# Kernel optimization log

Measured on AMD Instinct MI355X. Metric: run time of the kernel, lower is better.

Reference implementation:

```python
import jax, jax.numpy as jnp
import numpy as np

H = 1024
N_HEAD = 16
HEAD = H // N_HEAD
EPS = 1e-12


def setup_inputs() -> dict:
    key = jax.random.key(0)
    ks = jax.random.split(key, 12)
    B, S = 2, 2048
    scale = 1.0 / np.sqrt(H)
    inp = {
        "pre_out": jax.random.normal(ks[0], (B, S, H), dtype=jnp.float32),
        "att_mask": jnp.ones((B, 1, 1, S), dtype=jnp.float32),
        "Wq": jax.random.normal(ks[1], (H, H), dtype=jnp.float32) * scale,
        "bq": jnp.zeros((H,), dtype=jnp.float32),
        "Wk": jax.random.normal(ks[2], (H, H), dtype=jnp.float32) * scale,
        "bk": jnp.zeros((H,), dtype=jnp.float32),
        "Wv": jax.random.normal(ks[3], (H, H), dtype=jnp.float32) * scale,
        "bv": jnp.zeros((H,), dtype=jnp.float32),
        "Wo": jax.random.normal(ks[4], (H, H), dtype=jnp.float32) * scale,
        "bo": jnp.zeros((H,), dtype=jnp.float32),
        "ln_w": jnp.ones((H,), dtype=jnp.float32),
        "ln_b": jnp.zeros((H,), dtype=jnp.float32),
    }
    return inp


def _heads(x):
    # [B,S,H] -> [B,n_head,S,head]
    B, S, _ = x.shape
    return x.reshape(B, S, N_HEAD, HEAD).transpose(0, 2, 1, 3)


def _layernorm(x, w, b):
    u = jnp.mean(x, axis=-1, keepdims=True)
    s = jnp.mean((x - u) ** 2, axis=-1, keepdims=True)
    return w * ((x - u) / jnp.sqrt(s + EPS)) + b


def reference(pre_out, att_mask, Wq, bq, Wk, bk, Wv, bv, Wo, bo, ln_w, ln_b):
    B, S, _ = pre_out.shape
    # torch Linear: y = x @ W.T + b
    Q = _heads(pre_out @ Wq.T + bq)
    K = _heads(pre_out @ Wk.T + bk)
    V = _heads(pre_out @ Wv.T + bv)
    scores = jnp.einsum('bhqd,bhkd->bhqk', Q, K) / np.sqrt(HEAD)
    scores = scores + (1.0 - att_mask) * -10000.0
    prob = jax.nn.softmax(scores, axis=-1)  # eval mode: no dropout
    att = jnp.einsum('bhqk,bhkd->bhqd', prob, V)
    att = att.transpose(0, 2, 1, 3).reshape(B, S, H)
    out = att @ Wo.T + bo
    return _layernorm(pre_out + out, ln_w, ln_b)
```

## Files before the change

### kernel.cpp

```cpp
#include <hip/hip_runtime.h>
#include <math.h>

typedef unsigned short u16;
typedef float floatx4 __attribute__((ext_vector_type(4)));
typedef __bf16 bf16x8 __attribute__((ext_vector_type(8)));
typedef u16 u16x4 __attribute__((ext_vector_type(4)));

#define BB 2
#define SS 2048
#define HH 1024
#define NHEAD 16

__device__ __forceinline__ u16 f2bf(float f) {
  union { float f; unsigned u; } a; a.f = f;
  unsigned r = a.u + 0x7fffu + ((a.u >> 16) & 1u);
  return (u16)(r >> 16);
}

__device__ __forceinline__ u16 bfbits(float f) {
  union { __bf16 h; u16 u; } c; c.h = (__bf16)f; return c.u;
}

__device__ __forceinline__ unsigned cvtpk(float lo, float hi) {
  unsigned r;
  asm("v_cvt_pk_bf16_f32 %0, %1, %2" : "=v"(r) : "v"(lo), "v"(hi));
  return r;
}

__device__ __forceinline__ void gload16(const u16* g, u16* l) {
  __builtin_amdgcn_global_load_lds((const __attribute__((address_space(1))) void*)g,
                                   (__attribute__((address_space(3))) void*)l, 16, 0, 0);
}

__device__ __forceinline__ void fencebar() {
  asm volatile("" ::: "memory");
  __builtin_amdgcn_s_barrier();
  asm volatile("" ::: "memory");
}

__global__ __launch_bounds__(256) void cvt_all(
    const float* __restrict__ X, const float* __restrict__ Wq, const float* __restrict__ Wk,
    const float* __restrict__ Wv, const float* __restrict__ Wo, const float* __restrict__ mask,
    u16* __restrict__ Xb, u16* __restrict__ Wqb, u16* __restrict__ Wkb,
    u16* __restrict__ Wvb, u16* __restrict__ Wob, float* __restrict__ B2) {
  int i = blockIdx.x * 256 + threadIdx.x;
  if (i >= (2 << 20)) {
    int off = i - (2 << 20);
    float4 m = ((const float4*)mask)[off];
    float4 o;
    o.x = (1.0f - m.x) * (-10000.0f * 1.44269504f);
    o.y = (1.0f - m.y) * (-10000.0f * 1.44269504f);
    o.z = (1.0f - m.z) * (-10000.0f * 1.44269504f);
    o.w = (1.0f - m.w) * (-10000.0f * 1.44269504f);
    ((float4*)B2)[off] = o;
    return;
  }
  const float* src; u16* dst; int off;
  if (i < (1 << 20)) { src = X; dst = Xb; off = i; }
  else {
    int j = i - (1 << 20);
    int m = j >> 18; off = j & ((1 << 18) - 1);
    src = (m == 0) ? Wq : (m == 1) ? Wk : (m == 2) ? Wv : Wo;
    dst = (m == 0) ? Wqb : (m == 1) ? Wkb : (m == 2) ? Wvb : Wob;
  }
  float4 v = ((const float4*)src)[off];
  u16x4 p; p.x = f2bf(v.x); p.y = f2bf(v.y); p.z = f2bf(v.z); p.w = f2bf(v.w);
  ((u16x4*)dst)[off] = p;
}

__global__ __launch_bounds__(256) void qkv_gemm(
    const u16* __restrict__ X,
    const u16* __restrict__ Wq, const u16* __restrict__ Wk, const u16* __restrict__ Wv,
    const float* __restrict__ bq, const float* __restrict__ bk, const float* __restrict__ bv,
    u16* __restrict__ Qo, u16* __restrict__ Ko, u16* __restrict__ Vt) {
  __shared__ u16 As[2][128 * 32];
  __shared__ u16 Ws[2][128 * 32];

  const int tid = threadIdx.x;
  const int w = tid >> 6, lane = tid & 63, quad = lane >> 4, l15 = lane & 15;
  const int L = blockIdx.y * 24 + blockIdx.x;
  const int wid = (L & 7) * 96 + (L >> 3);
  const int bx = wid % 24, by = wid / 24;
  const int mat = bx >> 3;
  const int col0 = (bx & 7) * 128;
  const int row0 = by * 128;
  const u16* W = (mat == 0) ? Wq : (mat == 1) ? Wk : Wv;
  const float* bias = (mat == 0) ? bq : (mat == 1) ? bk : bv;

  const int c0 = tid, c1 = tid + 256;
  const int ar0 = c0 >> 2, al0 = ((c0 & 3) ^ (ar0 & 3)) * 8;
  const int ar1 = c1 >> 2, al1 = ((c1 & 3) ^ (ar1 & 3)) * 8;
  const u16* gA0 = X + (row0 + ar0) * HH + al0;
  const u16* gA1 = X + (row0 + ar1) * HH + al1;
  const u16* gW0 = W + (col0 + ar0) * HH + al0;
  const u16* gW1 = W + (col0 + ar1) * HH + al1;

  const int wm = (w >> 1) * 64, wn = (w & 1) * 64;
  const int sw = quad ^ (l15 & 3);
  const int aoff = (wm + l15) * 32 + sw * 8;
  const int boff = (wn + l15) * 32 + sw * 8;

  auto stage = [&](int buf, int k0) {
    gload16(gA0 + k0, As[buf] + c0 * 8);
    gload16(gA1 + k0, As[buf] + c1 * 8);
    gload16(gW0 + k0, Ws[buf] + c0 * 8);
    gload16(gW1 + k0, Ws[buf] + c1 * 8);
  };

  floatx4 acc[4][4];
#pragma unroll
  for (int i = 0; i < 4; i++)
#pragma unroll
    for (int j = 0; j < 4; j++) acc[i][j] = {0.f, 0.f, 0.f, 0.f};

  stage(0, 0);

  for (int kt = 0; kt < 32; kt++) {
    const int cur = kt & 1;
    if (kt < 31) {
      stage(cur ^ 1, (kt + 1) * 32);
      asm volatile("s_waitcnt vmcnt(4)" ::: "memory");
    } else {
      asm volatile("s_waitcnt vmcnt(0)" ::: "memory");
    }
    fencebar();

    bf16x8 af[4], bfr[4];
#pragma unroll
    for (int i = 0; i < 4; i++) af[i] = *(const bf16x8*)(As[cur] + aoff + i * 512);
#pragma unroll
    for (int j = 0; j < 4; j++) bfr[j] = *(const bf16x8*)(Ws[cur] + boff + j * 512);
    __builtin_amdgcn_s_setprio(1);
#pragma unroll
    for (int i = 0; i < 4; i++)
#pragma unroll
      for (int j = 0; j < 4; j++)
        acc[i][j] = __builtin_amdgcn_mfma_f32_16x16x32_bf16(af[i], bfr[j], acc[i][j], 0, 0, 0);
    __builtin_amdgcn_s_setprio(0);

    fencebar();
  }

  const int rb = row0 + wm + quad * 4;
  if (mat < 2) {
    u16* O = (mat == 0) ? Qo : Ko;
#pragma unroll
    for (int j = 0; j < 4; j++) {
      const int col = col0 + wn + j * 16 + l15;
      const float bj = bias[col];
#pragma unroll
      for (int i = 0; i < 4; i++) {
        const int r0 = rb + i * 16;
#pragma unroll
        for (int r = 0; r < 4; r++)
          O[(r0 + r) * HH + col] = bfbits(acc[i][j][r] + bj);
      }
    }
  } else {
#pragma unroll
    for (int j = 0; j < 4; j++) {
      const int col = col0 + wn + j * 16 + l15;
      const float bj = bias[col];
      const int h = col >> 6, d = col & 63;
#pragma unroll
      for (int i = 0; i < 4; i++) {
        const int m0 = rb + i * 16;
        const int b = m0 >> 11, s = m0 & 2047;
        u16x4 pk;
#pragma unroll
        for (int r = 0; r < 4; r++) pk[r] = bfbits(acc[i][j][r] + bj);
        *(u16x4*)(Vt + (((b * NHEAD + h) * 64 + d) * SS + s)) = pk;
      }
    }
  }
}

__global__ __launch_bounds__(256) void oproj_gemm(
    const u16* __restrict__ A, const u16* __restrict__ W,
    const float* __restrict__ bias, float* __restrict__ Y) {
  __shared__ u16 As[2][128 * 32];
  __shared__ u16 Ws[2][64 * 32];

  const int tid = threadIdx.x;
  const int w = tid >> 6, lane = tid & 63, quad = lane >> 4, l15 = lane & 15;
  const int L = blockIdx.y * 16 + blockIdx.x;
  const int wid = (L & 7) * 64 + (L >> 3);
  const int col0 = (wid & 15) * 64;
  const int row0 = (wid >> 4) * 128;

  const int c0 = tid, c1 = tid + 256;
  const int ar0 = c0 >> 2, al0 = ((c0 & 3) ^ (ar0 & 3)) * 8;
  const int ar1 = c1 >> 2, al1 = ((c1 & 3) ^ (ar1 & 3)) * 8;
  const u16* gA0 = A + (row0 + ar0) * HH + al0;
  const u16* gA1 = A + (row0 + ar1) * HH + al1;
  const u16* gW0 = W + (col0 + ar0) * HH + al0;

  const int wm = w * 32;
  const int sw = quad ^ (l15 & 3);
  const int aoff = (wm + l15) * 32 + sw * 8;
  const int boff = l15 * 32 + sw * 8;

  auto stage = [&](int buf, int k0) {
    gload16(gA0 + k0, As[buf] + c0 * 8);
    gload16(gA1 + k0, As[buf] + c1 * 8);
    gload16(gW0 + k0, Ws[buf] + c0 * 8);
  };

  floatx4 acc[2][4];
#pragma unroll
  for (int i = 0; i < 2; i++)
#pragma unroll
    for (int j = 0; j < 4; j++) acc[i][j] = {0.f, 0.f, 0.f, 0.f};

  stage(0, 0);

  for (int kt = 0; kt < 32; kt++) {
    const int cur = kt & 1;
    if (kt < 31) {
      stage(cur ^ 1, (kt + 1) * 32);
      asm volatile("s_waitcnt vmcnt(3)" ::: "memory");
    } else {
      asm volatile("s_waitcnt vmcnt(0)" ::: "memory");
    }
    fencebar();

    bf16x8 af[2], bfr[4];
#pragma unroll
    for (int i = 0; i < 2; i++) af[i] = *(const bf16x8*)(As[cur] + aoff + i * 512);
#pragma unroll
    for (int j = 0; j < 4; j++) bfr[j] = *(const bf16x8*)(Ws[cur] + boff + j * 512);
    __builtin_amdgcn_s_setprio(1);
#pragma unroll
    for (int i = 0; i < 2; i++)
#pragma unroll
      for (int j = 0; j < 4; j++)
        acc[i][j] = __builtin_amdgcn_mfma_f32_16x16x32_bf16(af[i], bfr[j], acc[i][j], 0, 0, 0);
    __builtin_amdgcn_s_setprio(0);

    fencebar();
  }

  const int rb = row0 + wm + quad * 4;
#pragma unroll
  for (int j = 0; j < 4; j++) {
    const int col = col0 + j * 16 + l15;
    const float bj = bias[col];
#pragma unroll
    for (int i = 0; i < 2; i++) {
      const int r0 = rb + i * 16;
#pragma unroll
      for (int r = 0; r < 4; r++)
        Y[(r0 + r) * HH + col] = acc[i][j][r] + bj;
    }
  }
}

#define QT 128

__global__ __launch_bounds__(512, 4) void attn_mfma(
    const u16* __restrict__ Q, const u16* __restrict__ K, const u16* __restrict__ Vt,
    const float* __restrict__ B2, u16* __restrict__ O) {
  __shared__ u16 SMEM[32768];
  u16* const UQ = SMEM;
  u16* const KB = SMEM + 8192;
  u16* const VB = SMEM + 20480;

  const int L = blockIdx.y * 16 + blockIdx.x;
  const int wid = (L & 7) * 64 + (L >> 3);
  const int qt = wid & 15, bh = wid >> 4;
  const int b = bh >> 4, h = bh & 15;
  const int tid = threadIdx.x;
  const int w = tid >> 6, lane = tid & 63, quad = lane >> 4, l15 = lane & 15;
  const int sw = l15 & 7;
  const int qg = w & 3;
  const int khalf = w >> 2;
  const int koff = khalf * 32;

  const int qbase  = (b * SS + qt * QT) * HH + h * 64;
  const int kvbase = (b * SS) * HH + h * 64;
  const int vtbase = (b * NHEAD + h) * 64 * SS;

  auto stage_kv = [&](int bi, int t) {
    const int c = tid;
    const int r = c >> 3, lc = (c & 7) ^ (r & 7);
    gload16(K + kvbase + (t * 64 + r) * HH + lc * 8, KB + bi * 4096 + c * 8);
    gload16(Vt + vtbase + r * SS + t * 64 + lc * 8, VB + bi * 4096 + c * 8);
  };

#pragma unroll
  for (int i = 0; i < 2; i++) {
    const int c = tid + i * 512;
    const int r = c >> 3, lc = (c & 7) ^ (r & 7);
    gload16(Q + qbase + r * HH + lc * 8, UQ + c * 8);
  }
  stage_kv(0, 0);
  stage_kv(1, 1);
  asm volatile("s_waitcnt vmcnt(4)" ::: "memory");
  fencebar();

  bf16x8 aQ[2][2];
#pragma unroll
  for (int mt = 0; mt < 2; mt++) {
    const u16* qr = UQ + (qg * 32 + mt * 16 + l15) * 64;
    aQ[mt][0] = *(const bf16x8*)(qr + ((quad ^ sw) * 8));
    aQ[mt][1] = *(const bf16x8*)(qr + (((4 + quad) ^ sw) * 8));
  }

  floatx4 o[2][4];
#pragma unroll
  for (int mt = 0; mt < 2; mt++)
#pragma unroll
    for (int j = 0; j < 4; j++) o[mt][j] = {0.f, 0.f, 0.f, 0.f};
  float lp[2] = {0.f, 0.f};

  const float* B2row = B2 + b * SS;

  const int vc0 = khalf * 4 + (quad >> 1);
  const int vsub = (quad & 1) * 4;

  for (int kt = 0; kt < 32; kt++) {
    const int cI = kt % 3;

    fencebar();

    const float* B2k = B2row + kt * 64 + koff;
    floatx4 bb[2];
    bb[0] = *(const floatx4*)(B2k + quad * 4);
    bb[1] = *(const floatx4*)(B2k + 16 + quad * 4);
    asm volatile("" ::: "memory");

    if (kt < 30) {
      stage_kv((kt + 2) % 3, kt + 2);
      asm volatile("s_waitcnt vmcnt(2)" ::: "memory");
    } else {
      asm volatile("s_waitcnt vmcnt(0)" ::: "memory");
    }

    const u16* Kc = KB + cI * 4096;
    const u16* Vc = VB + cI * 4096;

    floatx4 st[2][2];
    __builtin_amdgcn_s_setprio(1);
#pragma unroll
    for (int kb = 0; kb < 2; kb++) {
      const u16* kr = Kc + (koff + kb * 16 + l15) * 64;
      bf16x8 kf0 = *(const bf16x8*)(kr + ((quad ^ sw) * 8));
      bf16x8 kf1 = *(const bf16x8*)(kr + (((4 + quad) ^ sw) * 8));
#pragma unroll
      for (int mt = 0; mt < 2; mt++) {
        floatx4 z = {0.f, 0.f, 0.f, 0.f};
        z = __builtin_amdgcn_mfma_f32_16x16x32_bf16(kf0, aQ[mt][0], z, 0, 0, 0);
        st[mt][kb] = __builtin_amdgcn_mfma_f32_16x16x32_bf16(kf1, aQ[mt][1], z, 0, 0, 0);
      }
    }
    __builtin_amdgcn_s_setprio(0);

    bf16x8 pa[2];
#pragma unroll
    for (int mt = 0; mt < 2; mt++) {
      float pe[2][4];
#pragma unroll
      for (int kb = 0; kb < 2; kb++)
#pragma unroll
        for (int r = 0; r < 4; r++) {
          pe[kb][r] = __builtin_amdgcn_exp2f(st[mt][kb][r] * 0.180336880f + bb[kb][r]);
          lp[mt] += pe[kb][r];
        }
      union { unsigned wd[4]; bf16x8 v; } pu;
      pu.wd[0] = cvtpk(pe[0][0], pe[0][1]);
      pu.wd[1] = cvtpk(pe[0][2], pe[0][3]);
      pu.wd[2] = cvtpk(pe[1][0], pe[1][1]);
      pu.wd[3] = cvtpk(pe[1][2], pe[1][3]);
      pa[mt] = pu.v;
    }

    __builtin_amdgcn_s_setprio(1);
#pragma unroll
    for (int j = 0; j < 4; j++) {
      const u16* vrow = Vc + (j * 16 + l15) * 64 + vsub;
      union { u16x4 hh[2]; bf16x8 v; } vu;
      vu.hh[0] = *(const u16x4*)(vrow + ((vc0 ^ sw) * 8));
      vu.hh[1] = *(const u16x4*)(vrow + (((vc0 + 2) ^ sw) * 8));
#pragma unroll
      for (int mt = 0; mt < 2; mt++)
        o[mt][j] = __builtin_amdgcn_mfma_f32_16x16x32_bf16(pa[mt], vu.v, o[mt][j], 0, 0, 0);
    }
    __builtin_amdgcn_s_setprio(0);
  }

  fencebar();

#pragma unroll
  for (int mt = 0; mt < 2; mt++) {
    float v = lp[mt];
    v += __shfl_xor(v, 16);
    v += __shfl_xor(v, 32);
    lp[mt] = v;
  }

  float* const oS  = (float*)(SMEM + 8192);
  float* const lpS = (float*)SMEM;
  if (w >= 4) {
    float* pb = oS + (w - 4) * 2048;
#pragma unroll
    for (int mt = 0; mt < 2; mt++) {
#pragma unroll
      for (int j = 0; j < 4; j++)
#pragma unroll
        for (int r = 0; r < 4; r++)
          pb[(mt * 16 + quad * 4 + r) * 64 + j * 16 + l15] = o[mt][j][r];
      if (quad == 0) lpS[qg * 32 + mt * 16 + l15] = lp[mt];
    }
  }
  asm volatile("s_waitcnt lgkmcnt(0)" ::: "memory");
  fencebar();

  if (w < 4) {
    const float* pb = oS + w * 2048;
    float lpt[2];
#pragma unroll
    for (int mt = 0; mt < 2; mt++)
      lpt[mt] = lp[mt] + lpS[w * 32 + mt * 16 + l15];
#pragma unroll
    for (int mt = 0; mt < 2; mt++) {
      const int orow0 = b * SS + qt * QT + qg * 32 + mt * 16 + quad * 4;
#pragma unroll
      for (int r = 0; r < 4; r++) {
        const float inv = 1.0f / __shfl(lpt[mt], quad * 4 + r);
#pragma unroll
        for (int j = 0; j < 4; j++) {
          const float val = o[mt][j][r] + pb[(mt * 16 + quad * 4 + r) * 64 + j * 16 + l15];
          O[(orow0 + r) * HH + h * 64 + j * 16 + l15] = bfbits(val * inv);
        }
      }
    }
  }
}

__global__ __launch_bounds__(256) void add_layernorm(
    const float* __restrict__ x0, const float* __restrict__ y,
    const float* __restrict__ w, const float* __restrict__ b,
    float* __restrict__ out) {
  const int row = blockIdx.x * 4 + (threadIdx.x >> 6);
  const int l = threadIdx.x & 63;
  const float4* xr = (const float4*)(x0 + (size_t)row * HH);
  const float4* yr = (const float4*)(y + (size_t)row * HH);

  float4 v[4];
  float s = 0.f;
#pragma unroll
  for (int i = 0; i < 4; i++) {
    const float4 a = xr[l + i * 64];
    const float4 c = yr[l + i * 64];
    v[i].x = a.x + c.x; v[i].y = a.y + c.y;
    v[i].z = a.z + c.z; v[i].w = a.w + c.w;
    s += v[i].x + v[i].y + v[i].z + v[i].w;
  }
#pragma unroll
  for (int o = 1; o < 64; o <<= 1) s += __shfl_xor(s, o);
  const float mean = s * (1.0f / HH);

  float sq = 0.f;
#pragma unroll
  for (int i = 0; i < 4; i++) {
    const float dx = v[i].x - mean, dy = v[i].y - mean;
    const float dz = v[i].z - mean, dw = v[i].w - mean;
    sq += dx * dx + dy * dy + dz * dz + dw * dw;
  }
#pragma unroll
  for (int o = 1; o < 64; o <<= 1) sq += __shfl_xor(sq, o);
  const float inv = rsqrtf(sq * (1.0f / HH) + 1e-12f);

  float4* orow = (float4*)(out + (size_t)row * HH);
#pragma unroll
  for (int i = 0; i < 4; i++) {
    const float4 ww = ((const float4*)w)[l + i * 64];
    const float4 bb = ((const float4*)b)[l + i * 64];
    float4 o4;
    o4.x = ww.x * ((v[i].x - mean) * inv) + bb.x;
    o4.y = ww.y * ((v[i].y - mean) * inv) + bb.y;
    o4.z = ww.z * ((v[i].z - mean) * inv) + bb.z;
    o4.w = ww.w * ((v[i].w - mean) * inv) + bb.w;
    orow[l + i * 64] = o4;
  }
}

extern "C" void kernel_launch(void* const* d_in, const int* in_sizes, int n_in,
                              void* d_out, int out_size, void* d_ws, size_t ws_size,
                              hipStream_t stream) {
  const float* pre_out = (const float*)d_in[0];
  const float* mask    = (const float*)d_in[1];
  const float* Wq = (const float*)d_in[2];
  const float* bq = (const float*)d_in[3];
  const float* Wk = (const float*)d_in[4];
  const float* bk = (const float*)d_in[5];
  const float* Wv = (const float*)d_in[6];
  const float* bv = (const float*)d_in[7];
  const float* Wo = (const float*)d_in[8];
  const float* bo = (const float*)d_in[9];
  const float* ln_w = (const float*)d_in[10];
  const float* ln_b = (const float*)d_in[11];
  float* out = (float*)d_out;

  u16* Xb  = (u16*)d_ws;
  u16* Wqb = Xb + (4 << 20);
  u16* Wkb = Wqb + (1 << 20);
  u16* Wvb = Wkb + (1 << 20);
  u16* Wob = Wvb + (1 << 20);
  u16* Qb  = Wob + (1 << 20);
  u16* Kb  = Qb + (4 << 20);
  u16* Vtb = Kb + (4 << 20);
  u16* Ab  = Vtb + (4 << 20);
  float* Yb = (float*)(Ab + (4 << 20));
  float* B2 = Yb + (4 << 20);

  cvt_all<<<8196, 256, 0, stream>>>(pre_out, Wq, Wk, Wv, Wo, mask,
                                    Xb, Wqb, Wkb, Wvb, Wob, B2);

  qkv_gemm<<<dim3(24, 32), 256, 0, stream>>>(Xb, Wqb, Wkb, Wvb, bq, bk, bv, Qb, Kb, Vtb);

  attn_mfma<<<dim3(SS / QT, BB * NHEAD), 512, 0, stream>>>(Qb, Kb, Vtb, B2, Ab);

  oproj_gemm<<<dim3(16, 32), 256, 0, stream>>>(Ab, Wob, bo, Yb);

  add_layernorm<<<BB * SS / 4, 256, 0, stream>>>(pre_out, Yb, ln_w, ln_b, out);
}
```

Measured before the change: 207.9 us.

## Software-pipeline PV MFMA one tile behind QK and load Q directly to registers

```diff
diff --git a/kernel.cpp b/kernel.cpp
--- a/kernel.cpp
+++ b/kernel.cpp
@@ -260,10 +260,9 @@
 __global__ __launch_bounds__(512, 4) void attn_mfma(
     const u16* __restrict__ Q, const u16* __restrict__ K, const u16* __restrict__ Vt,
     const float* __restrict__ B2, u16* __restrict__ O) {
-  __shared__ u16 SMEM[32768];
-  u16* const UQ = SMEM;
-  u16* const KB = SMEM + 8192;
-  u16* const VB = SMEM + 20480;
+  __shared__ u16 SMEM[33024];
+  u16* const KB = SMEM;
+  u16* const VB = SMEM + 16384;
 
   const int L = blockIdx.y * 16 + blockIdx.x;
   const int wid = (L & 7) * 64 + (L >> 3);
@@ -287,24 +286,16 @@
     gload16(Vt + vtbase + r * SS + t * 64 + lc * 8, VB + bi * 4096 + c * 8);
   };
 
-#pragma unroll
-  for (int i = 0; i < 2; i++) {
-    const int c = tid + i * 512;
-    const int r = c >> 3, lc = (c & 7) ^ (r & 7);
-    gload16(Q + qbase + r * HH + lc * 8, UQ + c * 8);
+  bf16x8 aQ[2][2];
+#pragma unroll
+  for (int mt = 0; mt < 2; mt++) {
+    const u16* qr = Q + qbase + (qg * 32 + mt * 16 + l15) * HH;
+    aQ[mt][0] = *(const bf16x8*)(qr + quad * 8);
+    aQ[mt][1] = *(const bf16x8*)(qr + (4 + quad) * 8);
   }
   stage_kv(0, 0);
   stage_kv(1, 1);
-  asm volatile("s_waitcnt vmcnt(4)" ::: "memory");
-  fencebar();
-
-  bf16x8 aQ[2][2];
-#pragma unroll
-  for (int mt = 0; mt < 2; mt++) {
-    const u16* qr = UQ + (qg * 32 + mt * 16 + l15) * 64;
-    aQ[mt][0] = *(const bf16x8*)(qr + ((quad ^ sw) * 8));
-    aQ[mt][1] = *(const bf16x8*)(qr + (((4 + quad) ^ sw) * 8));
-  }
+  asm volatile("s_waitcnt vmcnt(2)" ::: "memory");
 
   floatx4 o[2][4];
 #pragma unroll
@@ -318,9 +309,9 @@
   const int vc0 = khalf * 4 + (quad >> 1);
   const int vsub = (quad & 1) * 4;
 
+  bf16x8 pa[2];
+
   for (int kt = 0; kt < 32; kt++) {
-    const int cI = kt % 3;
-
     fencebar();
 
     const float* B2k = B2row + kt * 64 + koff;
@@ -330,14 +321,13 @@
     asm volatile("" ::: "memory");
 
     if (kt < 30) {
-      stage_kv((kt + 2) % 3, kt + 2);
+      stage_kv((kt + 2) & 3, kt + 2);
       asm volatile("s_waitcnt vmcnt(2)" ::: "memory");
     } else {
       asm volatile("s_waitcnt vmcnt(0)" ::: "memory");
     }
 
-    const u16* Kc = KB + cI * 4096;
-    const u16* Vc = VB + cI * 4096;
+    const u16* Kc = KB + (kt & 3) * 4096;
 
     floatx4 st[2][2];
     __builtin_amdgcn_s_setprio(1);
@@ -353,9 +343,22 @@
         st[mt][kb] = __builtin_amdgcn_mfma_f32_16x16x32_bf16(kf1, aQ[mt][1], z, 0, 0, 0);
       }
     }
+
+    if (kt) {
+      const u16* Vp = VB + ((kt - 1) & 3) * 4096;
+#pragma unroll
+      for (int j = 0; j < 4; j++) {
+        const u16* vrow = Vp + (j * 16 + l15) * 64 + vsub;
+        union { u16x4 hh[2]; bf16x8 v; } vu;
+        vu.hh[0] = *(const u16x4*)(vrow + ((vc0 ^ sw) * 8));
+        vu.hh[1] = *(const u16x4*)(vrow + (((vc0 + 2) ^ sw) * 8));
+#pragma unroll
+        for (int mt = 0; mt < 2; mt++)
+          o[mt][j] = __builtin_amdgcn_mfma_f32_16x16x32_bf16(pa[mt], vu.v, o[mt][j], 0, 0, 0);
+      }
+    }
     __builtin_amdgcn_s_setprio(0);
 
-    bf16x8 pa[2];
 #pragma unroll
     for (int mt = 0; mt < 2; mt++) {
       float pe[2][4];
@@ -373,11 +376,14 @@
       pu.wd[3] = cvtpk(pe[1][2], pe[1][3]);
       pa[mt] = pu.v;
     }
-
+  }
+
+  {
+    const u16* Vp = VB + (31 & 3) * 4096;
     __builtin_amdgcn_s_setprio(1);
 #pragma unroll
     for (int j = 0; j < 4; j++) {
-      const u16* vrow = Vc + (j * 16 + l15) * 64 + vsub;
+      const u16* vrow = Vp + (j * 16 + l15) * 64 + vsub;
       union { u16x4 hh[2]; bf16x8 v; } vu;
       vu.hh[0] = *(const u16x4*)(vrow + ((vc0 ^ sw) * 8));
       vu.hh[1] = *(const u16x4*)(vrow + (((vc0 + 2) ^ sw) * 8));
@@ -398,8 +404,8 @@
     lp[mt] = v;
   }
 
-  float* const oS  = (float*)(SMEM + 8192);
-  float* const lpS = (float*)SMEM;
+  float* const oS  = (float*)SMEM;
+  float* const lpS = (float*)(SMEM + 32768);
   if (w >= 4) {
     float* pb = oS + (w - 4) * 2048;
 #pragma unroll
```

New measurement: 205.8 us. Within noise of the previous version (-1.0%).
